# Kernel optimization log

Hardware: AMD Instinct MI355X
Metric: run time of the kernel (lower is better)

The kernel has to match this reference:

```python
import jax, jax.numpy as jnp
import numpy as np

N, F, D = 4096, 32, 16      # nodes, channels, irrep dim for L<=3 (1+3+5+7)
E = 65536                    # edges (avg degree 16)
S = 64                       # species
R = 8                        # radial basis size
AVG = 16.0                   # avg_num_neighbors
L_SLICES = ((0, 1), (1, 4), (4, 9), (9, 16))   # per-l blocks of the 16-dim irrep axis
IR_OUT_REPS = np.array([1, 3])                 # output irreps 0e (dim 1) + 1o (dim 3)
MIX_REPS = np.array([1, 3, 5, 7])              # per-l scalar mix broadcast over m


def _sph(v):
    # real spherical harmonics l=1..3 of normalized vectors (4pi-normalized), [E,15]
    r2 = jnp.sum(v * v, axis=-1, keepdims=True)
    u = v / jnp.sqrt(jnp.where(r2 == 0.0, 1.0, r2))
    x, y, z = u[:, 0], u[:, 1], u[:, 2]
    s3, s5, s7 = 3.0 ** 0.5, 5.0 ** 0.5, 7.0 ** 0.5
    s15, s42, s70, s105 = 15.0 ** 0.5, 42.0 ** 0.5, 70.0 ** 0.5, 105.0 ** 0.5
    Y1 = [s3 * x, s3 * y, s3 * z]
    Y2 = [s15 * x * y, s15 * y * z, 0.5 * s5 * (3 * z * z - 1), s15 * x * z, 0.5 * s15 * (x * x - y * y)]
    Y3 = [0.25 * s70 * y * (3 * x * x - y * y), s105 * x * y * z, 0.25 * s42 * y * (5 * z * z - 1),
          0.5 * s7 * z * (5 * z * z - 3), 0.25 * s42 * x * (5 * z * z - 1),
          0.5 * s105 * z * (x * x - y * y), 0.25 * s70 * x * (x * x - 3 * y * y)]
    return jnp.stack(Y1 + Y2 + Y3, axis=-1)


def _per_l_linear(xs, W):
    # channel mixing within each l block: xs [N,C,16], W [4,C,Fout] -> [N,Fout,16]
    return jnp.concatenate([jnp.einsum('nci,cf->nfi', xs[:, :, a:b], W[l])
                            for l, (a, b) in enumerate(L_SLICES)], axis=-1)


def setup_inputs() -> dict:
    key = jax.random.key(0)
    ks = jax.random.split(key, 17)
    rs = np.random.RandomState(0)
    # sparse CG-like tensor-product / symmetric-contraction basis tensors (fixed constants)
    cg = (rs.randn(D, 15, D) * (rs.rand(D, 15, D) < 0.08)).astype(np.float32)
    u3 = (rs.randn(D, D, D, 4) * (rs.rand(D, D, D, 4) < 0.05)).astype(np.float32)
    u2 = (rs.randn(D, D, 4) * (rs.rand(D, D, 4) < 0.15)).astype(np.float32)
    u1 = (rs.randn(D, 4) * (rs.rand(D, 4) < 0.4)).astype(np.float32)

    def g(k, shape, s):
        return jax.random.normal(k, shape, dtype=jnp.float32) * s

    return {
        'node_feats': g(ks[0], (N, F, D), 1.0),
        'vectors': g(ks[1], (E, 3), 1.0),
        'radial_embedding': jax.random.uniform(ks[2], (E, R), dtype=jnp.float32),
        'W_up': g(ks[3], (4, F, F), F ** -0.5),
        'CG': jnp.asarray(cg),
        'W_r1': g(ks[4], (R, 64), R ** -0.5),
        'W_r2': g(ks[5], (64, 64), 64 ** -0.5),
        'W_r3': g(ks[6], (64, 64), 64 ** -0.5),
        'W_r4': g(ks[7], (64, 2 * F * 4), 64 ** -0.5),
        'W_down': g(ks[8], (4, 2 * F, F), (2 * F) ** -0.5),
        'U3': jnp.asarray(u3),
        'U2': jnp.asarray(u2),
        'U1': jnp.asarray(u1),
        'w3': g(ks[9], (S, 2, F), 1.0),
        'w2': g(ks[10], (S, 2, F), 1.0),
        'w1': g(ks[11], (S, 2, F), 1.0),
        'W_sc': g(ks[12], (2, S, F, F), F ** -0.5),
        'W_out': g(ks[13], (2, F, F), F ** -0.5),
        'node_species': jax.random.randint(ks[14], (N,), 0, S, dtype=jnp.int32),
        'senders': jax.random.randint(ks[15], (E,), 0, N, dtype=jnp.int32),
        'receivers': jax.random.randint(ks[16], (E,), 0, N, dtype=jnp.int32),
    }


def _forward(node_feats, vectors, radial_embedding, W_up, CG, W_r1, W_r2, W_r3, W_r4,
             W_down, U3, U2, U1, w3, w2, w1, W_sc, W_out,
             node_species, senders, receivers):
    # linear_up
    x = _per_l_linear(node_feats, W_up)                              # [N,F,16]
    # message passing convolution
    fs = x[senders]                                                  # gather [E,F,16]
    Y = _sph(vectors)                                                # [E,15]
    M = jnp.einsum('ej,ijk->eik', Y, CG)                             # per-edge TP operator [E,16,16]
    tp = jnp.einsum('efi,eik->efk', fs, M)                           # [E,F,16]
    msg = jnp.concatenate([fs, tp], axis=1)                          # [E,2F,16]
    h = jax.nn.silu(radial_embedding @ W_r1)
    h = jax.nn.silu(h @ W_r2)
    h = jax.nn.silu(h @ W_r3)
    mix = (h @ W_r4).reshape(E, 2 * F, 4)                            # per-(channel,l) scalar
    mix = jnp.repeat(mix, MIX_REPS, axis=-1, total_repeat_length=D)  # [E,2F,16]
    msg = msg * mix
    agg = jax.ops.segment_sum(msg, receivers, num_segments=N) / jnp.sqrt(AVG)
    y = _per_l_linear(agg, W_down) / jnp.sqrt(AVG)                   # linear_down [N,F,16]
    # symmetric contraction (correlation 3) with species-indexed weights
    def expand(w):  # [S,2,F] -> per-node per-output-irrep-dim scalar [N,F,4]
        return jnp.repeat(jnp.transpose(w[node_species], (0, 2, 1)), IR_OUT_REPS,
                          axis=-1, total_repeat_length=4)
    w3e, w2e, w1e = expand(w3), expand(w2), expand(w1)
    T = jnp.einsum('abji,ncj->ncabi', U3, y) * w3e[:, :, None, None, :]  # [N,F,16,16,4]
    T = T + U2[None, None] * w2e[:, :, None, None, :]
    T = jnp.einsum('ncaji,ncj->ncai', T, y)                              # [N,F,16,4]
    T = T + U1[None, None] * w1e[:, :, None, :]
    B = jnp.einsum('ncji,ncj->nci', T, y)                                # [N,F,4]
    # output linear (per output irrep) + species-indexed skip connection
    o = jnp.concatenate([jnp.einsum('nci,cf->nfi', B[:, :, :1], W_out[0]),
                         jnp.einsum('nci,cf->nfi', B[:, :, 1:4], W_out[1])], axis=-1)
    sc = jnp.concatenate([jnp.einsum('nci,ncf->nfi', x[:, :, :1], W_sc[0][node_species]),
                          jnp.einsum('nci,ncf->nfi', x[:, :, 1:4], W_sc[1][node_species])], axis=-1)
    return (o + sc).reshape(N, F * 4)


def reference(node_feats, vectors, radial_embedding, W_up, CG, W_r1, W_r2, W_r3, W_r4,
              W_down, U3, U2, U1, w3, w2, w1, W_sc, W_out,
              node_species, senders, receivers):
    return _forward(node_feats, vectors, radial_embedding, W_up, CG, W_r1, W_r2, W_r3, W_r4,
                    W_down, U3, U2, U1, w3, w2, w1, W_sc, W_out,
                    node_species, senders, receivers)
```

## Files before the change

### kernel.cpp

```cpp
#include <hip/hip_runtime.h>
#include <hip/hip_fp16.h>
#include <math.h>

#define NN 4096
#define FF 32
#define DD 16
#define EE 65536

__device__ __forceinline__ int l_of(int i){ return (i==0)?0:(i<4)?1:(i<9)?2:3; }
__device__ __forceinline__ float silu(float v){ return v/(1.f+expf(-v)); }

__global__ __launch_bounds__(512) void k_x(const float* __restrict__ feats,
        const float* __restrict__ Wup, float* __restrict__ x){
  __shared__ float sF[4*512];
  __shared__ float sW[4*FF*FF];
  int n0 = blockIdx.x*4, t = threadIdx.x;
  #pragma unroll
  for(int q=0;q<4;q++) sF[q*512+t] = feats[(size_t)(n0+q)*512 + t];
  for (int k=t;k<4*FF*FF;k+=512) sW[k]=Wup[k];
  __syncthreads();
  int f = t>>4, i = t&15;
  const float* W = &sW[l_of(i)*FF*FF];
  #pragma unroll
  for(int q=0;q<4;q++){
    float a=0.f;
    #pragma unroll
    for (int c=0;c<FF;c++) a += sF[q*512 + c*DD+i]*W[c*FF+f];
    x[(size_t)(n0+q)*512 + t] = a;
  }
}

__global__ __launch_bounds__(256) void k_YM(const float* __restrict__ vec,
    const float* __restrict__ CG, const int* __restrict__ epos,
    __half* __restrict__ M_h){
  int t = threadIdx.x;
  int e = blockIdx.x*16 + (t>>4);
  int i = t&15;
  float vx=vec[(size_t)e*3+0], vy=vec[(size_t)e*3+1], vz=vec[(size_t)e*3+2];
  float r2=vx*vx+vy*vy+vz*vz;
  float inv = (r2==0.f)?1.f:rsqrtf(r2);
  float X=vx*inv, Y=vy*inv, Z=vz*inv;
  const float s3=1.7320508075688772f, s5=2.23606797749979f, s7=2.6457513110645907f;
  const float s15=3.872983346207417f, s42=6.48074069840786f, s70=8.366600265340756f, s105=10.246950765959598f;
  float y[15];
  y[0]=s3*X; y[1]=s3*Y; y[2]=s3*Z;
  y[3]=s15*X*Y; y[4]=s15*Y*Z; y[5]=0.5f*s5*(3.f*Z*Z-1.f); y[6]=s15*X*Z; y[7]=0.5f*s15*(X*X-Y*Y);
  y[8]=0.25f*s70*Y*(3.f*X*X-Y*Y); y[9]=s105*X*Y*Z; y[10]=0.25f*s42*Y*(5.f*Z*Z-1.f);
  y[11]=0.5f*s7*Z*(5.f*Z*Z-3.f); y[12]=0.25f*s42*X*(5.f*Z*Z-1.f);
  y[13]=0.5f*s105*Z*(X*X-Y*Y); y[14]=0.25f*s70*X*(X*X-3.f*Y*Y);
  float m[16];
  #pragma unroll
  for(int k=0;k<16;k++) m[k]=0.f;
  const float* cgr = CG + i*240;
  #pragma unroll
  for(int j=0;j<15;j++){
    float yj = y[j];
    #pragma unroll
    for(int q=0;q<4;q++){
      float4 c4 = *(const float4*)&cgr[j*16 + q*4];
      m[q*4+0]+=yj*c4.x; m[q*4+1]+=yj*c4.y; m[q*4+2]+=yj*c4.z; m[q*4+3]+=yj*c4.w;
    }
  }
  size_t slot = (size_t)epos[e];
  __half2* dst = (__half2*)&M_h[slot*256 + i*16];
  #pragma unroll
  for(int q=0;q<8;q++) dst[q] = __floats2half2_rn(m[2*q], m[2*q+1]);
}

__global__ __launch_bounds__(256) void k_mix(const float* __restrict__ rad,
    const float* __restrict__ W1, const float* __restrict__ W2,
    const float* __restrict__ W3, const float* __restrict__ W4,
    const int* __restrict__ epos, __half* __restrict__ mix_h){
  __shared__ float sRadT[8*68];
  __shared__ float sW1[8*64];
  __shared__ float sHA[64*68];
  __shared__ float sHB[64*68];
  int t = threadIdx.x;
  int be = blockIdx.x*64;
  for (int k=t;k<8*64;k+=256) sW1[k]=W1[k];
  for (int idx=t; idx<64*8; idx+=256){ int e=idx>>3, k=idx&7; sRadT[k*68+e]=rad[(size_t)(be+e)*8+k]; }
  __syncthreads();
  int e0 = (t>>4)*4, j0 = (t&15)*4;
  {
    float acc[4][4];
    #pragma unroll
    for(int a=0;a<4;a++){ acc[a][0]=0;acc[a][1]=0;acc[a][2]=0;acc[a][3]=0; }
    #pragma unroll
    for(int k=0;k<8;k++){
      float4 h = *(const float4*)&sRadT[k*68+e0];
      float4 w = *(const float4*)&sW1[k*64+j0];
      acc[0][0]+=h.x*w.x; acc[0][1]+=h.x*w.y; acc[0][2]+=h.x*w.z; acc[0][3]+=h.x*w.w;
      acc[1][0]+=h.y*w.x; acc[1][1]+=h.y*w.y; acc[1][2]+=h.y*w.z; acc[1][3]+=h.y*w.w;
      acc[2][0]+=h.z*w.x; acc[2][1]+=h.z*w.y; acc[2][2]+=h.z*w.z; acc[2][3]+=h.z*w.w;
      acc[3][0]+=h.w*w.x; acc[3][1]+=h.w*w.y; acc[3][2]+=h.w*w.z; acc[3][3]+=h.w*w.w;
    }
    #pragma unroll
    for(int b=0;b<4;b++){
      float4 v; v.x=silu(acc[0][b]); v.y=silu(acc[1][b]); v.z=silu(acc[2][b]); v.w=silu(acc[3][b]);
      *(float4*)&sHA[(j0+b)*68+e0] = v;
    }
  }
  __syncthreads();
  {
    float acc[4][4];
    #pragma unroll
    for(int a=0;a<4;a++){ acc[a][0]=0;acc[a][1]=0;acc[a][2]=0;acc[a][3]=0; }
    for(int k=0;k<64;k++){
      float4 h = *(const float4*)&sHA[k*68+e0];
      float4 w = *(const float4*)&W2[k*64+j0];
      acc[0][0]+=h.x*w.x; acc[0][1]+=h.x*w.y; acc[0][2]+=h.x*w.z; acc[0][3]+=h.x*w.w;
      acc[1][0]+=h.y*w.x; acc[1][1]+=h.y*w.y; acc[1][2]+=h.y*w.z; acc[1][3]+=h.y*w.w;
      acc[2][0]+=h.z*w.x; acc[2][1]+=h.z*w.y; acc[2][2]+=h.z*w.z; acc[2][3]+=h.z*w.w;
      acc[3][0]+=h.w*w.x; acc[3][1]+=h.w*w.y; acc[3][2]+=h.w*w.z; acc[3][3]+=h.w*w.w;
    }
    #pragma unroll
    for(int b=0;b<4;b++){
      float4 v; v.x=silu(acc[0][b]); v.y=silu(acc[1][b]); v.z=silu(acc[2][b]); v.w=silu(acc[3][b]);
      *(float4*)&sHB[(j0+b)*68+e0] = v;
    }
  }
  __syncthreads();
  {
    float acc[4][4];
    #pragma unroll
    for(int a=0;a<4;a++){ acc[a][0]=0;acc[a][1]=0;acc[a][2]=0;acc[a][3]=0; }
    for(int k=0;k<64;k++){
      float4 h = *(const float4*)&sHB[k*68+e0];
      float4 w = *(const float4*)&W3[k*64+j0];
      acc[0][0]+=h.x*w.x; acc[0][1]+=h.x*w.y; acc[0][2]+=h.x*w.z; acc[0][3]+=h.x*w.w;
      acc[1][0]+=h.y*w.x; acc[1][1]+=h.y*w.y; acc[1][2]+=h.y*w.z; acc[1][3]+=h.y*w.w;
      acc[2][0]+=h.z*w.x; acc[2][1]+=h.z*w.y; acc[2][2]+=h.z*w.z; acc[2][3]+=h.z*w.w;
      acc[3][0]+=h.w*w.x; acc[3][1]+=h.w*w.y; acc[3][2]+=h.w*w.z; acc[3][3]+=h.w*w.w;
    }
    #pragma unroll
    for(int b=0;b<4;b++){
      float4 v; v.x=silu(acc[0][b]); v.y=silu(acc[1][b]); v.z=silu(acc[2][b]); v.w=silu(acc[3][b]);
      *(float4*)&sHA[(j0+b)*68+e0] = v;
    }
  }
  __syncthreads();
  {
    int cc0 = (t&63)*4, g = t>>6;
    float acc[4][4][4];
    #pragma unroll
    for(int r=0;r<4;r++)
      #pragma unroll
      for(int a=0;a<4;a++){ acc[r][a][0]=0;acc[r][a][1]=0;acc[r][a][2]=0;acc[r][a][3]=0; }
    for(int k=0;k<64;k++){
      float4 w = *(const float4*)&W4[k*256+cc0];
      #pragma unroll
      for(int r=0;r<4;r++){
        float4 h = *(const float4*)&sHA[k*68 + (g+4*r)*4];
        acc[r][0][0]+=h.x*w.x; acc[r][0][1]+=h.x*w.y; acc[r][0][2]+=h.x*w.z; acc[r][0][3]+=h.x*w.w;
        acc[r][1][0]+=h.y*w.x; acc[r][1][1]+=h.y*w.y; acc[r][1][2]+=h.y*w.z; acc[r][1][3]+=h.y*w.w;
        acc[r][2][0]+=h.z*w.x; acc[r][2][1]+=h.z*w.y; acc[r][2][2]+=h.z*w.z; acc[r][2][3]+=h.z*w.w;
        acc[r][3][0]+=h.w*w.x; acc[r][3][1]+=h.w*w.y; acc[r][3][2]+=h.w*w.z; acc[r][3][3]+=h.w*w.w;
      }
    }
    #pragma unroll
    for(int r=0;r<4;r++)
      #pragma unroll
      for(int a=0;a<4;a++){
        int e = (g+4*r)*4 + a;
        size_t ep = (size_t)epos[be+e];
        __half2* dst = (__half2*)&mix_h[ep*256 + cc0];
        dst[0]=__floats2half2_rn(acc[r][a][0], acc[r][a][1]);
        dst[1]=__floats2half2_rn(acc[r][a][2], acc[r][a][3]);
      }
  }
}

__global__ void k_zero(int* cnt){ int t=blockIdx.x*256+threadIdx.x; if(t<NN) cnt[t]=0; }
__global__ void k_count(const int* __restrict__ recv, int* cnt, int* pos){
  int e=blockIdx.x*256+threadIdx.x; pos[e]=atomicAdd(&cnt[recv[e]],1); }
__global__ __launch_bounds__(256) void k_scan(const int* __restrict__ cnt, int* __restrict__ off){
  __shared__ int sums[256]; __shared__ int bases[256];
  int t=threadIdx.x;
  int local[16]; int s=0;
  #pragma unroll
  for(int k=0;k<16;k++){ local[k]=cnt[t*16+k]; s+=local[k]; }
  sums[t]=s; __syncthreads();
  if(t==0){ int a=0; for(int q=0;q<256;q++){ bases[q]=a; a+=sums[q]; } }
  __syncthreads();
  int acc=bases[t];
  #pragma unroll
  for(int k=0;k<16;k++){ off[t*16+k]=acc; acc+=local[k]; }
  if(t==255) off[NN]=acc;
}
__global__ void k_fill(const int* __restrict__ recv, const int* __restrict__ off,
                       const int* __restrict__ pos, int* __restrict__ elist){
  int e=blockIdx.x*256+threadIdx.x; elist[off[recv[e]]+pos[e]]=e; }

__global__ __launch_bounds__(256) void k_sort(const int* __restrict__ senders,
    const int* __restrict__ off, const int* __restrict__ elist,
    int* __restrict__ epos, int* __restrict__ ssend){
  __shared__ int buf[4][256];
  int t=threadIdx.x, w=t>>6, l=t&63;
  int n = blockIdx.x*4 + w;
  int base = off[n];
  int deg = off[n+1]-base; if (deg>256) deg=256;
  for(int d=l; d<deg; d+=64) buf[w][d]=elist[base+d];
  __syncthreads();
  for(int d=l; d<deg; d+=64){
    int v=buf[w][d]; int r=0;
    for(int q=0;q<deg;q++) r += (buf[w][q]<v);
    epos[v] = base + r;
    ssend[base+r] = senders[v];
  }
}

__global__ __launch_bounds__(256) void k_compact(const float* __restrict__ U3,
    const float* __restrict__ U2, const float* __restrict__ U1,
    int* u3i, float* u3v, int* u2i, float* u2v, int* u1i, float* u1v, int* uoff){
  const float* src; int n; int* oi; float* ov; int slot=blockIdx.x;
  if(slot==0){src=U3;n=16384;oi=u3i;ov=u3v;}
  else if(slot==1){src=U2;n=1024;oi=u2i;ov=u2v;}
  else {src=U1;n=64;oi=u1i;ov=u1v;}
  __shared__ int cnts[256][4]; __shared__ int bases[256][4];
  int t=threadIdx.x;
  int chunk=(n+255)/256;
  int lo=t*chunk, hi=min(n,lo+chunk); if(lo>n) lo=n;
  int c0=0,c1=0,c2=0,c3=0;
  for(int q=lo;q<hi;q++) if(src[q]!=0.f){
    int i=q&3;
    if(i==0)c0++; else if(i==1)c1++; else if(i==2)c2++; else c3++;
  }
  cnts[t][0]=c0; cnts[t][1]=c1; cnts[t][2]=c2; cnts[t][3]=c3;
  __syncthreads();
  if(t==0){
    int a=0;
    for(int i=0;i<4;i++){ uoff[slot*5+i]=a;
      for(int q=0;q<256;q++){ bases[q][i]=a; a+=cnts[q][i]; } }
    uoff[slot*5+4]=a;
  }
  __syncthreads();
  int w0=bases[t][0], w1_=bases[t][1], w2_=bases[t][2], w3_=bases[t][3];
  for(int q=lo;q<hi;q++){ float v=src[q]; if(v!=0.f){
    int i=q&3;
    if(i==0){ oi[w0]=q; ov[w0]=v; w0++; }
    else if(i==1){ oi[w1_]=q; ov[w1_]=v; w1_++; }
    else if(i==2){ oi[w2_]=q; ov[w2_]=v; w2_++; }
    else { oi[w3_]=q; ov[w3_]=v; w3_++; }
  } }
}

__global__ __launch_bounds__(256) void k_gather(
    const float* __restrict__ x, const __half* __restrict__ mix_h,
    const __half* __restrict__ M_h,
    const int* __restrict__ off, const int* __restrict__ ssend,
    float* __restrict__ agg)
{
  __shared__ __align__(16) float sP[4096];
  __shared__ int sSnd[256];
  int t=threadIdx.x, w=t>>6, l=t&63, lc=l&31, kh=(l>>5)*8;
  bool lohalf = (l>>5)==0;
  int n = blockIdx.x;
  int base = off[n];
  int deg  = off[n+1]-base; if (deg>256) deg=256;
  for (int d=t; d<deg; d+=256) sSnd[d]=ssend[base+d];
  __syncthreads();

  float a0=0,a1=0,a2=0,a3=0,a4=0,a5=0,a6=0,a7=0;
  float b0=0,b1=0,b2=0,b3=0,b4=0,b5=0,b6=0,b7=0;

  float4 pa,pb,pc,pd;
  if (w < deg){
    int snd0 = sSnd[w];
    const float* xr = x + (size_t)snd0*512 + lc*16;
    pa = *(const float4*)&xr[0];
    pb = *(const float4*)&xr[4];
    pc = *(const float4*)&xr[8];
    pd = *(const float4*)&xr[12];
  }

  for (int d=w; d<deg; d+=4){
    int slot = base+d;
    float4 xa=pa, xb=pb, xc=pc, xd=pd;
    int dn = d+4;
    if (dn < deg){
      int snd2 = sSnd[dn];
      const float* xr2 = x + (size_t)snd2*512 + lc*16;
      pa = *(const float4*)&xr2[0];
      pb = *(const float4*)&xr2[4];
      pc = *(const float4*)&xr2[8];
      pd = *(const float4*)&xr2[12];
    }
    const float* mrowf = (const float*)(mix_h + (size_t)slot*256);
    float2 mraw = *(const float2*)&mrowf[lc*2];
    float2 traw = *(const float2*)&mrowf[64 + lc*2];
    float2 mf01 = __half22float2(__builtin_bit_cast(__half2, mraw.x));
    float2 mf23 = __half22float2(__builtin_bit_cast(__half2, mraw.y));
    float2 mt01 = __half22float2(__builtin_bit_cast(__half2, traw.x));
    float2 mt23 = __half22float2(__builtin_bit_cast(__half2, traw.y));
    const __half* Mrow = M_h + (size_t)slot*256 + kh;
    float t0=0,t1=0,t2=0,t3=0,t4=0,t5=0,t6=0,t7=0;
#define ACCM(F,IOFF) { \
    float4 mr = *(const float4*)&Mrow[(IOFF)*16]; \
    float2 m01=__half22float2(__builtin_bit_cast(__half2, mr.x)); \
    float2 m23=__half22float2(__builtin_bit_cast(__half2, mr.y)); \
    float2 m45=__half22float2(__builtin_bit_cast(__half2, mr.z)); \
    float2 m67=__half22float2(__builtin_bit_cast(__half2, mr.w)); \
    t0+=(F)*m01.x; t1+=(F)*m01.y; t2+=(F)*m23.x; t3+=(F)*m23.y; \
    t4+=(F)*m45.x; t5+=(F)*m45.y; t6+=(F)*m67.x; t7+=(F)*m67.y; }
    ACCM(xa.x,0)  ACCM(xa.y,1)  ACCM(xa.z,2)  ACCM(xa.w,3)
    ACCM(xb.x,4)  ACCM(xb.y,5)  ACCM(xb.z,6)  ACCM(xb.w,7)
    ACCM(xc.x,8)  ACCM(xc.y,9)  ACCM(xc.z,10) ACCM(xc.w,11)
    ACCM(xd.x,12) ACCM(xd.y,13) ACCM(xd.z,14) ACCM(xd.w,15)
#undef ACCM
    float mg0 = lohalf ? mf01.x : mf23.x;
    float mg1 = lohalf ? mf01.y : mf23.y;
    float mg4 = lohalf ? mf23.x : mf23.y;
    float ng0 = lohalf ? mt01.x : mt23.x;
    float ng1 = lohalf ? mt01.y : mt23.y;
    float ng4 = lohalf ? mt23.x : mt23.y;
    float f0 = lohalf ? xa.x : xc.x;
    float f1 = lohalf ? xa.y : xc.y;
    float f2 = lohalf ? xa.z : xc.z;
    float f3 = lohalf ? xa.w : xc.w;
    float f4 = lohalf ? xb.x : xd.x;
    float f5 = lohalf ? xb.y : xd.y;
    float f6 = lohalf ? xb.z : xd.z;
    float f7 = lohalf ? xb.w : xd.w;
    a0 += f0*mg0;  b0 += t0*ng0;
    a1 += f1*mg1;  b1 += t1*ng1;
    a2 += f2*mg1;  b2 += t2*ng1;
    a3 += f3*mg1;  b3 += t3*ng1;
    a4 += f4*mg4;  b4 += t4*ng4;
    a5 += f5*mg4;  b5 += t5*ng4;
    a6 += f6*mg4;  b6 += t6*ng4;
    a7 += f7*mg4;  b7 += t7*ng4;
  }

  int ibF = w*1024 + lc*16 + kh;
  int ibT = w*1024 + (32+lc)*16 + kh;
  sP[ibF+0]=a0; sP[ibF+1]=a1; sP[ibF+2]=a2; sP[ibF+3]=a3;
  sP[ibF+4]=a4; sP[ibF+5]=a5; sP[ibF+6]=a6; sP[ibF+7]=a7;
  sP[ibT+0]=b0; sP[ibT+1]=b1; sP[ibT+2]=b2; sP[ibT+3]=b3;
  sP[ibT+4]=b4; sP[ibT+5]=b5; sP[ibT+6]=b6; sP[ibT+7]=b7;
  __syncthreads();
  for (int idx=t; idx<1024; idx+=256)
    agg[(size_t)n*1024 + idx] = sP[idx]+sP[1024+idx]+sP[2048+idx]+sP[3072+idx];
}

__global__ __launch_bounds__(256) void k_tail(
    const float* __restrict__ agg, const float* __restrict__ x,
    const float* __restrict__ Wdown,
    const int* __restrict__ u3i, const float* __restrict__ u3v,
    const int* __restrict__ u2i, const float* __restrict__ u2v,
    const int* __restrict__ u1i, const float* __restrict__ u1v,
    const int* __restrict__ uoff,
    const float* __restrict__ w3, const float* __restrict__ w2,
    const float* __restrict__ w1,
    const float* __restrict__ Wsc, const float* __restrict__ Wout,
    const int* __restrict__ species,
    float* __restrict__ out)
{
  __shared__ float sAgg[4096];
  __shared__ float sy[2048];
  __shared__ float sPart[2048];

  int n0 = blockIdx.x*4, t = threadIdx.x;
  #pragma unroll
  for(int q=0;q<16;q++) sAgg[q*256+t] = agg[(size_t)n0*1024 + q*256 + t];
  __syncthreads();

  {
    int nq=t>>6, ii=t&15, f0=((t>>4)&3)*8;
    const float* W = Wdown + l_of(ii)*2048;
    float s0=0,s1=0,s2=0,s3=0,s4=0,s5=0,s6=0,s7=0;
    for(int c=0;c<64;c++){
      float a = sAgg[nq*1024 + c*16 + ii];
      float4 wva = *(const float4*)&W[c*32+f0];
      float4 wvb = *(const float4*)&W[c*32+f0+4];
      s0+=a*wva.x; s1+=a*wva.y; s2+=a*wva.z; s3+=a*wva.w;
      s4+=a*wvb.x; s5+=a*wvb.y; s6+=a*wvb.z; s7+=a*wvb.w;
    }
    float* yo = &sy[nq*512 + ii*32 + f0];
    yo[0]=s0*0.0625f; yo[1]=s1*0.0625f; yo[2]=s2*0.0625f; yo[3]=s3*0.0625f;
    yo[4]=s4*0.0625f; yo[5]=s5*0.0625f; yo[6]=s6*0.0625f; yo[7]=s7*0.0625f;
  }
  __syncthreads();

  float* sXn = sAgg;
  float* sB  = sAgg + 2048;
  #pragma unroll
  for(int q=0;q<8;q++){ int idx=q*256+t;
    sXn[idx] = x[(size_t)(n0+(idx>>9))*512 + (idx&511)]; }

  {
    int p = __builtin_amdgcn_readfirstlane(t>>6);
    int l = t&63, nq = l>>4, c0 = (l&15)*2;
    int spec = species[n0+nq];
    const float* syn = &sy[nq*512 + c0];
    #pragma unroll
    for(int i=0;i<4;i++){
      float r3x=0.f, r3y=0.f;
      #pragma unroll 2
      for(int q=uoff[i]+p; q<uoff[i+1]; q+=4){
        int id=u3i[q]; float v=u3v[q];
        int a=(id>>10)&15, b=(id>>6)&15, j=(id>>2)&15;
        float2 ya=*(const float2*)&syn[a*32];
        float2 yb=*(const float2*)&syn[b*32];
        float2 yj=*(const float2*)&syn[j*32];
        r3x += v*ya.x*yb.x*yj.x;
        r3y += v*ya.y*yb.y*yj.y;
      }
      float r2x=0.f, r2y=0.f;
      #pragma unroll 2
      for(int q=uoff[5+i]+p; q<uoff[5+i+1]; q+=4){
        int id=u2i[q]; float v=u2v[q];
        int a=(id>>6)&15, b=(id>>2)&15;
        float2 ya=*(const float2*)&syn[a*32];
        float2 yb=*(const float2*)&syn[b*32];
        r2x += v*ya.x*yb.x;
        r2y += v*ya.y*yb.y;
      }
      float r1x=0.f, r1y=0.f;
      for(int q=uoff[10+i]+p; q<uoff[10+i+1]; q+=4){
        int id=u1i[q]; float v=u1v[q];
        int a=(id>>2)&15;
        float2 ya=*(const float2*)&syn[a*32];
        r1x += v*ya.x;
        r1y += v*ya.y;
      }
      int wo = spec*64 + ((i==0)?0:32) + c0;
      float2 wa = *(const float2*)&w3[wo];
      float2 wb = *(const float2*)&w2[wo];
      float2 wc = *(const float2*)&w1[wo];
      float2 res;
      res.x = r3x*wa.x + r2x*wb.x + r1x*wc.x;
      res.y = r3y*wa.y + r2y*wb.y + r1y*wc.y;
      *(float2*)&sPart[p*512 + i*128 + nq*32 + c0] = res;
    }
  }
  __syncthreads();

  #pragma unroll
  for(int q=0;q<2;q++){
    int idx=q*256+t;
    int nq=idx>>7, rem=idx&127, c=rem>>2, i=rem&3;
    int o = i*128 + nq*32 + c;
    sB[nq*128 + c*4 + i] = sPart[o]+sPart[512+o]+sPart[1024+o]+sPart[1536+o];
  }
  __syncthreads();

  #pragma unroll
  for(int q=0;q<2;q++){
    int idx=q*256+t;
    int nq=idx>>7, rem=idx&127, f=rem>>2, i3=rem&3;
    int sp2 = species[n0+nq];
    int sel = (i3==0)?0:1;
    const float* Wo = Wout + sel*1024;
    const float* Ws = Wsc + (size_t)(sel*64+sp2)*1024;
    float o=0.f, sc=0.f;
    for(int c2=0;c2<32;c2++){
      o  += sB[nq*128 + c2*4 + i3]*Wo[c2*32+f];
      sc += sXn[nq*512 + c2*16 + i3]*Ws[c2*32+f];
    }
    out[(size_t)(n0+nq)*128 + f*4 + i3] = o + sc;
  }
}

extern "C" void kernel_launch(void* const* d_in, const int* in_sizes, int n_in,
                              void* d_out, int out_size, void* d_ws, size_t ws_size,
                              hipStream_t stream){
  (void)in_sizes; (void)n_in; (void)out_size; (void)ws_size;
  const float* feats = (const float*)d_in[0];
  const float* vec   = (const float*)d_in[1];
  const float* rad   = (const float*)d_in[2];
  const float* Wup   = (const float*)d_in[3];
  const float* CG    = (const float*)d_in[4];
  const float* Wr1   = (const float*)d_in[5];
  const float* Wr2   = (const float*)d_in[6];
  const float* Wr3   = (const float*)d_in[7];
  const float* Wr4   = (const float*)d_in[8];
  const float* Wdown = (const float*)d_in[9];
  const float* U3    = (const float*)d_in[10];
  const float* U2    = (const float*)d_in[11];
  const float* U1    = (const float*)d_in[12];
  const float* w3    = (const float*)d_in[13];
  const float* w2    = (const float*)d_in[14];
  const float* w1    = (const float*)d_in[15];
  const float* Wsc   = (const float*)d_in[16];
  const float* Wout  = (const float*)d_in[17];
  const int* species = (const int*)d_in[18];
  const int* senders = (const int*)d_in[19];
  const int* recv    = (const int*)d_in[20];
  float* out = (float*)d_out;

  char* w = (char*)d_ws;
  float* x     = (float*)w;  w += (size_t)NN*512*4;
  __half* mixh = (__half*)w; w += (size_t)EE*256*2;
  __half* Mh   = (__half*)w; w += (size_t)EE*256*2;
  float* agg   = (float*)w;  w += (size_t)NN*1024*4;
  int* cnt    = (int*)w;    w += (size_t)NN*4;
  int* off    = (int*)w;    w += (size_t)(NN+1)*4;
  int* pos    = (int*)w;    w += (size_t)EE*4;
  int* elist  = (int*)w;    w += (size_t)EE*4;
  int* epos   = (int*)w;    w += (size_t)EE*4;
  int* ssend  = (int*)w;    w += (size_t)EE*4;
  int* u3i    = (int*)w;    w += 16384*4;
  float* u3v  = (float*)w;  w += 16384*4;
  int* u2i    = (int*)w;    w += 1024*4;
  float* u2v  = (float*)w;  w += 1024*4;
  int* u1i    = (int*)w;    w += 64*4;
  float* u1v  = (float*)w;  w += 64*4;
  int* uoff   = (int*)w;    w += 16*4;

  k_compact<<<3,256,0,stream>>>(U3,U2,U1,u3i,u3v,u2i,u2v,u1i,u1v,uoff);
  k_x<<<NN/4,512,0,stream>>>(feats,Wup,x);
  k_zero<<<NN/256,256,0,stream>>>(cnt);
  k_count<<<EE/256,256,0,stream>>>(recv,cnt,pos);
  k_scan<<<1,256,0,stream>>>(cnt,off);
  k_fill<<<EE/256,256,0,stream>>>(recv,off,pos,elist);
  k_sort<<<NN/4,256,0,stream>>>(senders,off,elist,epos,ssend);
  k_YM<<<EE/16,256,0,stream>>>(vec,CG,epos,Mh);
  k_mix<<<EE/64,256,0,stream>>>(rad,Wr1,Wr2,Wr3,Wr4,epos,mixh);
  k_gather<<<NN,256,0,stream>>>(x,mixh,Mh,off,ssend,agg);
  k_tail<<<NN/4,256,0,stream>>>(agg,x,Wdown,u3i,u3v,u2i,u2v,u1i,u1v,uoff,
                                w3,w2,w1,Wsc,Wout,species,out);
}
```

Baseline: 315.2 us.

## Fuse graph preprocessing into cooperative kernel and merge YM into mix kernel

Replaces the separate compact, zero, count, scan, fill and sort kernels with a single cooperative kernel that uses grid-wide syncs between phases. The spherical-harmonic/CG edge projection moves from its own kernel into the tail of the radial-mix kernel. The aim is to cut launch overhead and inter-kernel gaps for the small preprocessing steps. It also raises the unroll factor of the sparse U3/U2 contraction loops in the tail kernel. The cost is grid-sync latency, a dependence on cooperative launch with a fixed grid of 256 blocks, and more register pressure in the mix kernel.

```diff
diff --git a/kernel.cpp b/kernel.cpp
--- a/kernel.cpp
+++ b/kernel.cpp
@@ -1,6 +1,9 @@
 #include <hip/hip_runtime.h>
 #include <hip/hip_fp16.h>
+#include <hip/hip_cooperative_groups.h>
 #include <math.h>
+
+namespace cg = cooperative_groups;
 
 #define NN 4096
 #define FF 32
@@ -30,47 +33,99 @@
   }
 }
 
-__global__ __launch_bounds__(256) void k_YM(const float* __restrict__ vec,
-    const float* __restrict__ CG, const int* __restrict__ epos,
-    __half* __restrict__ M_h){
-  int t = threadIdx.x;
-  int e = blockIdx.x*16 + (t>>4);
-  int i = t&15;
-  float vx=vec[(size_t)e*3+0], vy=vec[(size_t)e*3+1], vz=vec[(size_t)e*3+2];
-  float r2=vx*vx+vy*vy+vz*vz;
-  float inv = (r2==0.f)?1.f:rsqrtf(r2);
-  float X=vx*inv, Y=vy*inv, Z=vz*inv;
-  const float s3=1.7320508075688772f, s5=2.23606797749979f, s7=2.6457513110645907f;
-  const float s15=3.872983346207417f, s42=6.48074069840786f, s70=8.366600265340756f, s105=10.246950765959598f;
-  float y[15];
-  y[0]=s3*X; y[1]=s3*Y; y[2]=s3*Z;
-  y[3]=s15*X*Y; y[4]=s15*Y*Z; y[5]=0.5f*s5*(3.f*Z*Z-1.f); y[6]=s15*X*Z; y[7]=0.5f*s15*(X*X-Y*Y);
-  y[8]=0.25f*s70*Y*(3.f*X*X-Y*Y); y[9]=s105*X*Y*Z; y[10]=0.25f*s42*Y*(5.f*Z*Z-1.f);
-  y[11]=0.5f*s7*Z*(5.f*Z*Z-3.f); y[12]=0.25f*s42*X*(5.f*Z*Z-1.f);
-  y[13]=0.5f*s105*Z*(X*X-Y*Y); y[14]=0.25f*s70*X*(X*X-3.f*Y*Y);
-  float m[16];
-  #pragma unroll
-  for(int k=0;k<16;k++) m[k]=0.f;
-  const float* cgr = CG + i*240;
-  #pragma unroll
-  for(int j=0;j<15;j++){
-    float yj = y[j];
-    #pragma unroll
-    for(int q=0;q<4;q++){
-      float4 c4 = *(const float4*)&cgr[j*16 + q*4];
-      m[q*4+0]+=yj*c4.x; m[q*4+1]+=yj*c4.y; m[q*4+2]+=yj*c4.z; m[q*4+3]+=yj*c4.w;
-    }
-  }
-  size_t slot = (size_t)epos[e];
-  __half2* dst = (__half2*)&M_h[slot*256 + i*16];
-  #pragma unroll
-  for(int q=0;q<8;q++) dst[q] = __floats2half2_rn(m[2*q], m[2*q+1]);
+__global__ __launch_bounds__(256) void k_prep(
+    const float* __restrict__ U3, const float* __restrict__ U2, const float* __restrict__ U1,
+    int* __restrict__ u3i, float* __restrict__ u3v,
+    int* __restrict__ u2i, float* __restrict__ u2v,
+    int* __restrict__ u1i, float* __restrict__ u1v, int* __restrict__ uoff,
+    const int* __restrict__ recv, const int* __restrict__ senders,
+    int* __restrict__ cnt, int* __restrict__ off, int* __restrict__ pos,
+    int* __restrict__ elist, int* __restrict__ epos, int* __restrict__ ssend)
+{
+  cg::grid_group grid = cg::this_grid();
+  __shared__ int shmem[2048];
+  int t=threadIdx.x, b=blockIdx.x;
+  int gid = b*256+t;
+
+  if (gid < NN) cnt[gid] = 0;
+  if (b < 3){
+    const float* src; int nsz; int* oi; float* ov; int slot=b;
+    if(slot==0){src=U3;nsz=16384;oi=u3i;ov=u3v;}
+    else if(slot==1){src=U2;nsz=1024;oi=u2i;ov=u2v;}
+    else {src=U1;nsz=64;oi=u1i;ov=u1v;}
+    int (*cnts)[4]  = (int(*)[4])shmem;
+    int (*bases)[4] = (int(*)[4])(shmem+1024);
+    int chunk=(nsz+255)/256;
+    int lo=t*chunk, hi=min(nsz,lo+chunk); if(lo>nsz) lo=nsz;
+    int c0=0,c1=0,c2=0,c3=0;
+    for(int q=lo;q<hi;q++) if(src[q]!=0.f){
+      int i=q&3;
+      if(i==0)c0++; else if(i==1)c1++; else if(i==2)c2++; else c3++;
+    }
+    cnts[t][0]=c0; cnts[t][1]=c1; cnts[t][2]=c2; cnts[t][3]=c3;
+    __syncthreads();
+    if(t==0){
+      int a=0;
+      for(int i=0;i<4;i++){ uoff[slot*5+i]=a;
+        for(int q=0;q<256;q++){ bases[q][i]=a; a+=cnts[q][i]; } }
+      uoff[slot*5+4]=a;
+    }
+    __syncthreads();
+    int w0=bases[t][0], w1_=bases[t][1], w2_=bases[t][2], w3_=bases[t][3];
+    for(int q=lo;q<hi;q++){ float v=src[q]; if(v!=0.f){
+      int i=q&3;
+      if(i==0){ oi[w0]=q; ov[w0]=v; w0++; }
+      else if(i==1){ oi[w1_]=q; ov[w1_]=v; w1_++; }
+      else if(i==2){ oi[w2_]=q; ov[w2_]=v; w2_++; }
+      else { oi[w3_]=q; ov[w3_]=v; w3_++; }
+    } }
+  }
+  grid.sync();
+
+  pos[gid] = atomicAdd(&cnt[recv[gid]], 1);
+  grid.sync();
+
+  if (b==0){
+    int* sums = shmem; int* bss = shmem+256;
+    int local[16]; int s=0;
+    #pragma unroll
+    for(int k=0;k<16;k++){ local[k]=cnt[t*16+k]; s+=local[k]; }
+    sums[t]=s; __syncthreads();
+    if(t==0){ int a=0; for(int q=0;q<256;q++){ bss[q]=a; a+=sums[q]; } }
+    __syncthreads();
+    int acc=bss[t];
+    #pragma unroll
+    for(int k=0;k<16;k++){ off[t*16+k]=acc; acc+=local[k]; }
+    if(t==255) off[NN]=acc;
+  }
+  grid.sync();
+
+  elist[off[recv[gid]]+pos[gid]] = gid;
+  grid.sync();
+
+  {
+    int w=t>>6, l=t&63;
+    int* buf = shmem;
+    for (int n = b*4 + w; n < NN; n += 1024){
+      int base = off[n];
+      int deg = off[n+1]-base; if (deg>256) deg=256;
+      for(int d=l; d<deg; d+=64) buf[w*256+d]=elist[base+d];
+      for(int d=l; d<deg; d+=64){
+        int v=buf[w*256+d]; int r=0;
+        for(int q=0;q<deg;q++) r += (buf[w*256+q]<v);
+        epos[v] = base + r;
+        ssend[base+r] = senders[v];
+      }
+    }
+  }
 }
 
 __global__ __launch_bounds__(256) void k_mix(const float* __restrict__ rad,
     const float* __restrict__ W1, const float* __restrict__ W2,
     const float* __restrict__ W3, const float* __restrict__ W4,
-    const int* __restrict__ epos, __half* __restrict__ mix_h){
+    const int* __restrict__ epos, __half* __restrict__ mix_h,
+    const float* __restrict__ vec, const float* __restrict__ CG,
+    __half* __restrict__ M_h){
   __shared__ float sRadT[8*68];
   __shared__ float sW1[8*64];
   __shared__ float sHA[64*68];
@@ -168,80 +223,42 @@
         dst[1]=__floats2half2_rn(acc[r][a][2], acc[r][a][3]);
       }
   }
-}
-
-__global__ void k_zero(int* cnt){ int t=blockIdx.x*256+threadIdx.x; if(t<NN) cnt[t]=0; }
-__global__ void k_count(const int* __restrict__ recv, int* cnt, int* pos){
-  int e=blockIdx.x*256+threadIdx.x; pos[e]=atomicAdd(&cnt[recv[e]],1); }
-__global__ __launch_bounds__(256) void k_scan(const int* __restrict__ cnt, int* __restrict__ off){
-  __shared__ int sums[256]; __shared__ int bases[256];
-  int t=threadIdx.x;
-  int local[16]; int s=0;
-  #pragma unroll
-  for(int k=0;k<16;k++){ local[k]=cnt[t*16+k]; s+=local[k]; }
-  sums[t]=s; __syncthreads();
-  if(t==0){ int a=0; for(int q=0;q<256;q++){ bases[q]=a; a+=sums[q]; } }
-  __syncthreads();
-  int acc=bases[t];
-  #pragma unroll
-  for(int k=0;k<16;k++){ off[t*16+k]=acc; acc+=local[k]; }
-  if(t==255) off[NN]=acc;
-}
-__global__ void k_fill(const int* __restrict__ recv, const int* __restrict__ off,
-                       const int* __restrict__ pos, int* __restrict__ elist){
-  int e=blockIdx.x*256+threadIdx.x; elist[off[recv[e]]+pos[e]]=e; }
-
-__global__ __launch_bounds__(256) void k_sort(const int* __restrict__ senders,
-    const int* __restrict__ off, const int* __restrict__ elist,
-    int* __restrict__ epos, int* __restrict__ ssend){
-  __shared__ int buf[4][256];
-  int t=threadIdx.x, w=t>>6, l=t&63;
-  int n = blockIdx.x*4 + w;
-  int base = off[n];
-  int deg = off[n+1]-base; if (deg>256) deg=256;
-  for(int d=l; d<deg; d+=64) buf[w][d]=elist[base+d];
-  __syncthreads();
-  for(int d=l; d<deg; d+=64){
-    int v=buf[w][d]; int r=0;
-    for(int q=0;q<deg;q++) r += (buf[w][q]<v);
-    epos[v] = base + r;
-    ssend[base+r] = senders[v];
-  }
-}
-
-__global__ __launch_bounds__(256) void k_compact(const float* __restrict__ U3,
-    const float* __restrict__ U2, const float* __restrict__ U1,
-    int* u3i, float* u3v, int* u2i, float* u2v, int* u1i, float* u1v, int* uoff){
-  const float* src; int n; int* oi; float* ov; int slot=blockIdx.x;
-  if(slot==0){src=U3;n=16384;oi=u3i;ov=u3v;}
-  else if(slot==1){src=U2;n=1024;oi=u2i;ov=u2v;}
-  else {src=U1;n=64;oi=u1i;ov=u1v;}
-  __shared__ int cnts[256][4]; __shared__ int bases[256][4];
-  int t=threadIdx.x;
-  int chunk=(n+255)/256;
-  int lo=t*chunk, hi=min(n,lo+chunk); if(lo>n) lo=n;
-  int c0=0,c1=0,c2=0,c3=0;
-  for(int q=lo;q<hi;q++) if(src[q]!=0.f){
-    int i=q&3;
-    if(i==0)c0++; else if(i==1)c1++; else if(i==2)c2++; else c3++;
-  }
-  cnts[t][0]=c0; cnts[t][1]=c1; cnts[t][2]=c2; cnts[t][3]=c3;
-  __syncthreads();
-  if(t==0){
-    int a=0;
-    for(int i=0;i<4;i++){ uoff[slot*5+i]=a;
-      for(int q=0;q<256;q++){ bases[q][i]=a; a+=cnts[q][i]; } }
-    uoff[slot*5+4]=a;
-  }
-  __syncthreads();
-  int w0=bases[t][0], w1_=bases[t][1], w2_=bases[t][2], w3_=bases[t][3];
-  for(int q=lo;q<hi;q++){ float v=src[q]; if(v!=0.f){
-    int i=q&3;
-    if(i==0){ oi[w0]=q; ov[w0]=v; w0++; }
-    else if(i==1){ oi[w1_]=q; ov[w1_]=v; w1_++; }
-    else if(i==2){ oi[w2_]=q; ov[w2_]=v; w2_++; }
-    else { oi[w3_]=q; ov[w3_]=v; w3_++; }
-  } }
+  {
+    int i = t&15;
+    #pragma unroll
+    for(int qq=0;qq<4;qq++){
+      int e = be + (t>>4) + qq*16;
+      float vx=vec[(size_t)e*3+0], vy=vec[(size_t)e*3+1], vz=vec[(size_t)e*3+2];
+      float r2=vx*vx+vy*vy+vz*vz;
+      float inv = (r2==0.f)?1.f:rsqrtf(r2);
+      float X=vx*inv, Y=vy*inv, Z=vz*inv;
+      const float s3=1.7320508075688772f, s5=2.23606797749979f, s7=2.6457513110645907f;
+      const float s15=3.872983346207417f, s42=6.48074069840786f, s70=8.366600265340756f, s105=10.246950765959598f;
+      float y[15];
+      y[0]=s3*X; y[1]=s3*Y; y[2]=s3*Z;
+      y[3]=s15*X*Y; y[4]=s15*Y*Z; y[5]=0.5f*s5*(3.f*Z*Z-1.f); y[6]=s15*X*Z; y[7]=0.5f*s15*(X*X-Y*Y);
+      y[8]=0.25f*s70*Y*(3.f*X*X-Y*Y); y[9]=s105*X*Y*Z; y[10]=0.25f*s42*Y*(5.f*Z*Z-1.f);
+      y[11]=0.5f*s7*Z*(5.f*Z*Z-3.f); y[12]=0.25f*s42*X*(5.f*Z*Z-1.f);
+      y[13]=0.5f*s105*Z*(X*X-Y*Y); y[14]=0.25f*s70*X*(X*X-3.f*Y*Y);
+      float m[16];
+      #pragma unroll
+      for(int k=0;k<16;k++) m[k]=0.f;
+      const float* cgr = CG + i*240;
+      #pragma unroll
+      for(int j=0;j<15;j++){
+        float yj = y[j];
+        #pragma unroll
+        for(int q=0;q<4;q++){
+          float4 c4 = *(const float4*)&cgr[j*16 + q*4];
+          m[q*4+0]+=yj*c4.x; m[q*4+1]+=yj*c4.y; m[q*4+2]+=yj*c4.z; m[q*4+3]+=yj*c4.w;
+        }
+      }
+      size_t slot = (size_t)epos[e];
+      __half2* dst = (__half2*)&M_h[slot*256 + i*16];
+      #pragma unroll
+      for(int q=0;q<8;q++) dst[q] = __floats2half2_rn(m[2*q], m[2*q+1]);
+    }
+  }
 }
 
 __global__ __launch_bounds__(256) void k_gather(
@@ -395,7 +412,7 @@
     #pragma unroll
     for(int i=0;i<4;i++){
       float r3x=0.f, r3y=0.f;
-      #pragma unroll 2
+      #pragma unroll 4
       for(int q=uoff[i]+p; q<uoff[i+1]; q+=4){
         int id=u3i[q]; float v=u3v[q];
         int a=(id>>10)&15, b=(id>>6)&15, j=(id>>2)&15;
@@ -406,7 +423,7 @@
         r3y += v*ya.y*yb.y*yj.y;
       }
       float r2x=0.f, r2y=0.f;
-      #pragma unroll 2
+      #pragma unroll 4
       for(int q=uoff[5+i]+p; q<uoff[5+i+1]; q+=4){
         int id=u2i[q]; float v=u2v[q];
         int a=(id>>6)&15, b=(id>>2)&15;
@@ -507,15 +524,18 @@
   float* u1v  = (float*)w;  w += 64*4;
   int* uoff   = (int*)w;    w += 16*4;
 
-  k_compact<<<3,256,0,stream>>>(U3,U2,U1,u3i,u3v,u2i,u2v,u1i,u1v,uoff);
+  {
+    void* args[] = {
+      (void*)&U3, (void*)&U2, (void*)&U1,
+      (void*)&u3i, (void*)&u3v, (void*)&u2i, (void*)&u2v,
+      (void*)&u1i, (void*)&u1v, (void*)&uoff,
+      (void*)&recv, (void*)&senders,
+      (void*)&cnt, (void*)&off, (void*)&pos,
+      (void*)&elist, (void*)&epos, (void*)&ssend };
+    hipLaunchCooperativeKernel((void*)k_prep, dim3(256), dim3(256), args, 0, stream);
+  }
   k_x<<<NN/4,512,0,stream>>>(feats,Wup,x);
-  k_zero<<<NN/256,256,0,stream>>>(cnt);
-  k_count<<<EE/256,256,0,stream>>>(recv,cnt,pos);
-  k_scan<<<1,256,0,stream>>>(cnt,off);
-  k_fill<<<EE/256,256,0,stream>>>(recv,off,pos,elist);
-  k_sort<<<NN/4,256,0,stream>>>(senders,off,elist,epos,ssend);
-  k_YM<<<EE/16,256,0,stream>>>(vec,CG,epos,Mh);
-  k_mix<<<EE/64,256,0,stream>>>(rad,Wr1,Wr2,Wr3,Wr4,epos,mixh);
+  k_mix<<<EE/64,256,0,stream>>>(rad,Wr1,Wr2,Wr3,Wr4,epos,mixh,vec,CG,Mh);
   k_gather<<<NN,256,0,stream>>>(x,mixh,Mh,off,ssend,agg);
   k_tail<<<NN/4,256,0,stream>>>(agg,x,Wdown,u3i,u3v,u2i,u2v,u1i,u1v,uoff,
                                 w3,w2,w1,Wsc,Wout,species,out);
```

New measurement: 494.5 us. 56.9% more time.

## Fuse gather and tail kernels into one per-node kernel

Applied to the files above, without the earlier changes.

Merges the per-node edge gather with the down-projection, symmetric contraction and output linear stages into a single kernel with one block per node. The aggregated message stays in shared memory instead of going through a global agg buffer, which removes a write and reread and one kernel launch. In exchange the tail work is spread over one node per block rather than four, so per-block weight reloads and idle threads (only 128 active in the final stages) increase.

```diff
diff --git a/kernel.cpp b/kernel.cpp
--- a/kernel.cpp
+++ b/kernel.cpp
@@ -244,14 +244,29 @@
   } }
 }
 
-__global__ __launch_bounds__(256) void k_gather(
+__global__ __launch_bounds__(256) void k_fused(
     const float* __restrict__ x, const __half* __restrict__ mix_h,
     const __half* __restrict__ M_h,
     const int* __restrict__ off, const int* __restrict__ ssend,
-    float* __restrict__ agg)
+    const float* __restrict__ Wdown,
+    const int* __restrict__ u3i, const float* __restrict__ u3v,
+    const int* __restrict__ u2i, const float* __restrict__ u2v,
+    const int* __restrict__ u1i, const float* __restrict__ u1v,
+    const int* __restrict__ uoff,
+    const float* __restrict__ w3, const float* __restrict__ w2,
+    const float* __restrict__ w1,
+    const float* __restrict__ Wsc, const float* __restrict__ Wout,
+    const int* __restrict__ species,
+    float* __restrict__ out)
 {
   __shared__ __align__(16) float sP[4096];
   __shared__ int sSnd[256];
+  float* sAgg = sP;
+  float* sy   = sP + 1024;
+  float* sPrt = sP + 1536;
+  float* sXn  = sP + 2048;
+  float* sB   = sP + 2560;
+
   int t=threadIdx.x, w=t>>6, l=t&63, lc=l&31, kh=(l>>5)*8;
   bool lohalf = (l>>5)==0;
   int n = blockIdx.x;
@@ -339,125 +354,78 @@
   sP[ibT+4]=b4; sP[ibT+5]=b5; sP[ibT+6]=b6; sP[ibT+7]=b7;
   __syncthreads();
   for (int idx=t; idx<1024; idx+=256)
-    agg[(size_t)n*1024 + idx] = sP[idx]+sP[1024+idx]+sP[2048+idx]+sP[3072+idx];
-}
-
-__global__ __launch_bounds__(256) void k_tail(
-    const float* __restrict__ agg, const float* __restrict__ x,
-    const float* __restrict__ Wdown,
-    const int* __restrict__ u3i, const float* __restrict__ u3v,
-    const int* __restrict__ u2i, const float* __restrict__ u2v,
-    const int* __restrict__ u1i, const float* __restrict__ u1v,
-    const int* __restrict__ uoff,
-    const float* __restrict__ w3, const float* __restrict__ w2,
-    const float* __restrict__ w1,
-    const float* __restrict__ Wsc, const float* __restrict__ Wout,
-    const int* __restrict__ species,
-    float* __restrict__ out)
-{
-  __shared__ float sAgg[4096];
-  __shared__ float sy[2048];
-  __shared__ float sPart[2048];
-
-  int n0 = blockIdx.x*4, t = threadIdx.x;
-  #pragma unroll
-  for(int q=0;q<16;q++) sAgg[q*256+t] = agg[(size_t)n0*1024 + q*256 + t];
-  __syncthreads();
-
-  {
-    int nq=t>>6, ii=t&15, f0=((t>>4)&3)*8;
+    sAgg[idx] = sP[idx]+sP[1024+idx]+sP[2048+idx]+sP[3072+idx];
+  __syncthreads();
+
+  sXn[t]     = x[(size_t)n*512 + t];
+  sXn[256+t] = x[(size_t)n*512 + 256 + t];
+  {
+    int ii=t&15, f0=(t>>4)*2;
     const float* W = Wdown + l_of(ii)*2048;
-    float s0=0,s1=0,s2=0,s3=0,s4=0,s5=0,s6=0,s7=0;
+    float s0=0.f, s1=0.f;
     for(int c=0;c<64;c++){
-      float a = sAgg[nq*1024 + c*16 + ii];
-      float4 wva = *(const float4*)&W[c*32+f0];
-      float4 wvb = *(const float4*)&W[c*32+f0+4];
-      s0+=a*wva.x; s1+=a*wva.y; s2+=a*wva.z; s3+=a*wva.w;
-      s4+=a*wvb.x; s5+=a*wvb.y; s6+=a*wvb.z; s7+=a*wvb.w;
-    }
-    float* yo = &sy[nq*512 + ii*32 + f0];
-    yo[0]=s0*0.0625f; yo[1]=s1*0.0625f; yo[2]=s2*0.0625f; yo[3]=s3*0.0625f;
-    yo[4]=s4*0.0625f; yo[5]=s5*0.0625f; yo[6]=s6*0.0625f; yo[7]=s7*0.0625f;
-  }
-  __syncthreads();
-
-  float* sXn = sAgg;
-  float* sB  = sAgg + 2048;
-  #pragma unroll
-  for(int q=0;q<8;q++){ int idx=q*256+t;
-    sXn[idx] = x[(size_t)(n0+(idx>>9))*512 + (idx&511)]; }
-
+      float a = sAgg[c*16 + ii];
+      float2 wv = *(const float2*)&W[c*32+f0];
+      s0+=a*wv.x; s1+=a*wv.y;
+    }
+    sy[ii*32 + f0+0]=s0*0.0625f;
+    sy[ii*32 + f0+1]=s1*0.0625f;
+  }
+  __syncthreads();
+
+  int spec = species[n];
   {
     int p = __builtin_amdgcn_readfirstlane(t>>6);
-    int l = t&63, nq = l>>4, c0 = (l&15)*2;
-    int spec = species[n0+nq];
-    const float* syn = &sy[nq*512 + c0];
-    #pragma unroll
-    for(int i=0;i<4;i++){
-      float r3x=0.f, r3y=0.f;
-      #pragma unroll 2
+    int c = l&31, hi2 = l>>5;
+    const float* syc = &sy[c];
+    #pragma unroll
+    for(int ii2=0; ii2<2; ii2++){
+      int i = hi2*2 + ii2;
+      float r3=0.f;
+      #pragma unroll 4
       for(int q=uoff[i]+p; q<uoff[i+1]; q+=4){
         int id=u3i[q]; float v=u3v[q];
         int a=(id>>10)&15, b=(id>>6)&15, j=(id>>2)&15;
-        float2 ya=*(const float2*)&syn[a*32];
-        float2 yb=*(const float2*)&syn[b*32];
-        float2 yj=*(const float2*)&syn[j*32];
-        r3x += v*ya.x*yb.x*yj.x;
-        r3y += v*ya.y*yb.y*yj.y;
+        r3 += v*syc[a*32]*syc[b*32]*syc[j*32];
       }
-      float r2x=0.f, r2y=0.f;
-      #pragma unroll 2
+      float r2=0.f;
+      #pragma unroll 4
       for(int q=uoff[5+i]+p; q<uoff[5+i+1]; q+=4){
         int id=u2i[q]; float v=u2v[q];
         int a=(id>>6)&15, b=(id>>2)&15;
-        float2 ya=*(const float2*)&syn[a*32];
-        float2 yb=*(const float2*)&syn[b*32];
-        r2x += v*ya.x*yb.x;
-        r2y += v*ya.y*yb.y;
+        r2 += v*syc[a*32]*syc[b*32];
       }
-      float r1x=0.f, r1y=0.f;
+      float r1=0.f;
       for(int q=uoff[10+i]+p; q<uoff[10+i+1]; q+=4){
         int id=u1i[q]; float v=u1v[q];
         int a=(id>>2)&15;
-        float2 ya=*(const float2*)&syn[a*32];
-        r1x += v*ya.x;
-        r1y += v*ya.y;
+        r1 += v*syc[a*32];
       }
-      int wo = spec*64 + ((i==0)?0:32) + c0;
-      float2 wa = *(const float2*)&w3[wo];
-      float2 wb = *(const float2*)&w2[wo];
-      float2 wc = *(const float2*)&w1[wo];
-      float2 res;
-      res.x = r3x*wa.x + r2x*wb.x + r1x*wc.x;
-      res.y = r3y*wa.y + r2y*wb.y + r1y*wc.y;
-      *(float2*)&sPart[p*512 + i*128 + nq*32 + c0] = res;
-    }
-  }
-  __syncthreads();
-
-  #pragma unroll
-  for(int q=0;q<2;q++){
-    int idx=q*256+t;
-    int nq=idx>>7, rem=idx&127, c=rem>>2, i=rem&3;
-    int o = i*128 + nq*32 + c;
-    sB[nq*128 + c*4 + i] = sPart[o]+sPart[512+o]+sPart[1024+o]+sPart[1536+o];
-  }
-  __syncthreads();
-
-  #pragma unroll
-  for(int q=0;q<2;q++){
-    int idx=q*256+t;
-    int nq=idx>>7, rem=idx&127, f=rem>>2, i3=rem&3;
-    int sp2 = species[n0+nq];
+      int wo = spec*64 + ((i==0)?0:32) + c;
+      float wa = w3[wo], wb = w2[wo], wc = w1[wo];
+      sPrt[p*128 + i*32 + c] = r3*wa + r2*wb + r1*wc;
+    }
+  }
+  __syncthreads();
+
+  if (t<128){
+    int i=t>>5, c=t&31;
+    int o = i*32 + c;
+    sB[c*4 + i] = sPrt[o] + sPrt[128+o] + sPrt[256+o] + sPrt[384+o];
+  }
+  __syncthreads();
+
+  if (t<128){
+    int f=t>>2, i3=t&3;
     int sel = (i3==0)?0:1;
     const float* Wo = Wout + sel*1024;
-    const float* Ws = Wsc + (size_t)(sel*64+sp2)*1024;
+    const float* Ws = Wsc + (size_t)(sel*64+spec)*1024;
     float o=0.f, sc=0.f;
     for(int c2=0;c2<32;c2++){
-      o  += sB[nq*128 + c2*4 + i3]*Wo[c2*32+f];
-      sc += sXn[nq*512 + c2*16 + i3]*Ws[c2*32+f];
-    }
-    out[(size_t)(n0+nq)*128 + f*4 + i3] = o + sc;
+      o  += sB[c2*4 + i3]*Wo[c2*32+f];
+      sc += sXn[c2*16 + i3]*Ws[c2*32+f];
+    }
+    out[(size_t)n*128 + f*4 + i3] = o + sc;
   }
 }
 
@@ -492,7 +460,6 @@
   float* x     = (float*)w;  w += (size_t)NN*512*4;
   __half* mixh = (__half*)w; w += (size_t)EE*256*2;
   __half* Mh   = (__half*)w; w += (size_t)EE*256*2;
-  float* agg   = (float*)w;  w += (size_t)NN*1024*4;
   int* cnt    = (int*)w;    w += (size_t)NN*4;
   int* off    = (int*)w;    w += (size_t)(NN+1)*4;
   int* pos    = (int*)w;    w += (size_t)EE*4;
@@ -516,7 +483,7 @@
   k_sort<<<NN/4,256,0,stream>>>(senders,off,elist,epos,ssend);
   k_YM<<<EE/16,256,0,stream>>>(vec,CG,epos,Mh);
   k_mix<<<EE/64,256,0,stream>>>(rad,Wr1,Wr2,Wr3,Wr4,epos,mixh);
-  k_gather<<<NN,256,0,stream>>>(x,mixh,Mh,off,ssend,agg);
-  k_tail<<<NN/4,256,0,stream>>>(agg,x,Wdown,u3i,u3v,u2i,u2v,u1i,u1v,uoff,
-                                w3,w2,w1,Wsc,Wout,species,out);
-}
+  k_fused<<<NN,256,0,stream>>>(x,mixh,Mh,off,ssend,Wdown,
+                               u3i,u3v,u2i,u2v,u1i,u1v,uoff,
+                               w3,w2,w1,Wsc,Wout,species,out);
+}
```

After: 367.3 us. 16.6% more time.
